# Performance work log

Measured on AMD Instinct MI355X. Metric: run time of the kernel, lower is better.

## Reference

```python
import jax, jax.numpy as jnp
import numpy as np

N = 100000   # nodes
E = 1600000  # edges (before self-loops)
F_IN = 128
H = 64
G = 512      # graphs in batch


def _add_self_loops(edge_index, n):
    loop = jnp.arange(n, dtype=edge_index.dtype)
    src = jnp.concatenate([edge_index[0], loop])
    dst = jnp.concatenate([edge_index[1], loop])
    return src, dst


def _gcn_norm(src, dst, n):
    # PyG GCNConv: deg over targets with self-loops, norm = d^-1/2[src]*d^-1/2[dst]
    deg = jax.ops.segment_sum(jnp.ones_like(dst, dtype=jnp.float32), dst, num_segments=n)
    dinv = jnp.where(deg > 0, jax.lax.rsqrt(deg), 0.0)
    return dinv[src] * dinv[dst]


def _gcn_conv(x, src, dst, norm, W, b):
    xw = x @ W                                # [N, H]
    msg = xw[src] * norm[:, None]             # [E+N, H] gather + scale
    out = jax.ops.segment_sum(msg, dst, num_segments=x.shape[0])
    return out + b


def setup_inputs() -> dict:
    key = jax.random.key(0)
    ks = jax.random.split(key, 9)
    x = jax.random.normal(ks[0], (N, F_IN), dtype=jnp.float32)
    edge_index = jax.random.randint(ks[1], (2, E), 0, N, dtype=jnp.int32)
    batch = jnp.sort(jax.random.randint(ks[2], (N,), 0, G, dtype=jnp.int32))
    s1 = 1.0 / np.sqrt(F_IN)
    s2 = 1.0 / np.sqrt(H)
    W1 = jax.random.uniform(ks[3], (F_IN, H), jnp.float32, -s1, s1)
    b1 = jnp.zeros((H,), jnp.float32)
    W2 = jax.random.uniform(ks[4], (H, H), jnp.float32, -s2, s2)
    b2 = jnp.zeros((H,), jnp.float32)
    Wl = jax.random.uniform(ks[5], (H, 1), jnp.float32, -s2, s2)
    bl = jnp.zeros((1,), jnp.float32)
    return {"x": x, "edge_index": edge_index, "batch": batch,
            "W1": W1, "b1": b1, "W2": W2, "b2": b2, "Wl": Wl, "bl": bl}


def reference(x, edge_index, batch, W1, b1, W2, b2, Wl, bl):
    n = x.shape[0]
    src, dst = _add_self_loops(edge_index, n)
    norm = _gcn_norm(src, dst, n)
    h = jax.nn.relu(_gcn_conv(x, src, dst, norm, W1, b1))
    h = jax.nn.relu(_gcn_conv(h, src, dst, norm, W2, b2))
    # global mean pool over graphs
    sums = jax.ops.segment_sum(h, batch, num_segments=G)          # [G, H]
    cnt = jax.ops.segment_sum(jnp.ones((n,), jnp.float32), batch, num_segments=G)
    pooled = sums / jnp.maximum(cnt, 1.0)[:, None]
    return jax.nn.sigmoid(pooled @ Wl + bl)                        # [G, 1]
```

## Files before the change

### kernel.cpp

```cpp
#include <hip/hip_runtime.h>
#include <hip/hip_bf16.h>
#include <cmath>

#define F_IN 128
#define HDIM 64
#define NPB 256
#define NB1 1024

typedef __attribute__((ext_vector_type(8))) short bf16x8;
typedef __attribute__((ext_vector_type(4))) float f32x4;

__device__ __forceinline__ float bf2f(unsigned short u) {
    union { unsigned int i; float f; } v; v.i = ((unsigned int)u) << 16; return v.f;
}
__device__ __forceinline__ unsigned short f2bf(float f) {
    __hip_bfloat16 h = __float2bfloat16(f);
    union { __hip_bfloat16 h; unsigned short u; } c; c.h = h; return c.u;
}


__launch_bounds__(256)
__global__ void p0_count(const int* __restrict__ dst, int* __restrict__ blk_cnt,
                         int E, int nbuk, int chunk) {
    __shared__ int hist[512];
    int tid = threadIdx.x;
    for (int i = tid; i < nbuk; i += 256) hist[i] = 0;
    __syncthreads();
    int lo = blockIdx.x * chunk;
    int hi = min(E, lo + chunk);
    for (int e = lo + tid; e < hi; e += 256)
        atomicAdd(&hist[dst[e] >> 8], 1);
    __syncthreads();
    for (int i = tid; i < nbuk; i += 256)
        blk_cnt[i * NB1 + blockIdx.x] = hist[i];
}

__launch_bounds__(256)
__global__ void p_scan_blocks(int* __restrict__ blk_cnt, int* __restrict__ bucket_cnt) {
    __shared__ int sd[256];
    int b = blockIdx.x, tid = threadIdx.x;
    int4* row = (int4*)(blk_cnt + (size_t)b * NB1);
    int4 v = row[tid];
    int s0 = v.x, s1 = s0 + v.y, s2 = s1 + v.z, s3 = s2 + v.w;
    sd[tid] = s3;
    __syncthreads();
    for (int off = 1; off < 256; off <<= 1) {
        int a = (tid >= off) ? sd[tid - off] : 0;
        __syncthreads();
        sd[tid] += a;
        __syncthreads();
    }
    int base = sd[tid] - s3;
    int4 o;
    o.x = base; o.y = base + s0; o.z = base + s1; o.w = base + s2;
    row[tid] = o;
    if (tid == 255) bucket_cnt[b] = sd[255];
}

__global__ void p0_scan(const int* __restrict__ cnt, int* __restrict__ base, int nbuk) {
    __shared__ int sd[512];
    int tid = threadIdx.x;
    int v = (tid < nbuk) ? cnt[tid] : 0;
    sd[tid] = v;
    __syncthreads();
    for (int off = 1; off < 512; off <<= 1) {
        int a = (tid >= off) ? sd[tid - off] : 0;
        __syncthreads();
        sd[tid] += a;
        __syncthreads();
    }
    if (tid < nbuk) base[tid] = sd[tid] - v;
    if (tid == nbuk - 1) base[nbuk] = sd[tid];
}

__launch_bounds__(256)
__global__ void p1_place(const int* __restrict__ src, const int* __restrict__ dst,
                         const int* __restrict__ blk_cnt, const int* __restrict__ bucket_base,
                         int* __restrict__ pairs, int E, int nbuk, int chunk) {
    __shared__ int cur[512];
    int tid = threadIdx.x;
    for (int i = tid; i < nbuk; i += 256)
        cur[i] = bucket_base[i] + blk_cnt[i * NB1 + blockIdx.x];
    __syncthreads();
    int lo = blockIdx.x * chunk;
    int hi = min(E, lo + chunk);
    for (int e = lo + tid; e < hi; e += 256) {
        int d = dst[e];
        int pos = atomicAdd(&cur[d >> 8], 1);
        pairs[pos] = (src[e] << 8) | (d & 255);
    }
}

__launch_bounds__(256)
__global__ void p2_csr(const int* __restrict__ pairs, const int* __restrict__ base,
                       float* __restrict__ dinv, int* __restrict__ col,
                       int4* __restrict__ slot_hdr, int n) {
    __shared__ int dl[256];
    __shared__ int sc[256];
    __shared__ int cur[256];
    __shared__ int h64[64];
    __shared__ int s64[64];
    int b = blockIdx.x, tid = threadIdx.x;
    int nlo = b << 8;
    int eb = base[b], ee = base[b + 1];
    dl[tid] = 0;
    if (tid < 64) h64[tid] = 0;
    __syncthreads();
    for (int e = eb + tid; e < ee; e += 256)
        atomicAdd(&dl[pairs[e] & 255], 1);
    __syncthreads();
    int d0 = dl[tid];
    sc[tid] = d0;
    __syncthreads();
    for (int off = 1; off < 256; off <<= 1) {
        int a = (tid >= off) ? sc[tid - off] : 0;
        __syncthreads();
        sc[tid] += a;
        __syncthreads();
    }
    int excl = sc[tid] - d0;
    int node = nlo + tid;
    float dv = rsqrtf((float)(d0 + 1));
    if (node < n) dinv[node] = dv;
    cur[tid] = eb + excl;
    int bin = min(d0, 63);
    atomicAdd(&h64[bin], 1);
    __syncthreads();
    if (tid == 0) { int run = 0; for (int i = 0; i < 64; ++i) { s64[i] = run; run += h64[i]; } }
    __syncthreads();
    if (tid < 64) h64[tid] = 0;
    __syncthreads();
    int pos = s64[bin] + atomicAdd(&h64[bin], 1);
    int4 hdr;
    hdr.x = (node < n) ? node : 0x7fffffff;
    hdr.y = eb + excl;
    hdr.z = d0;
    hdr.w = __float_as_int(dv);
    slot_hdr[nlo + pos] = hdr;
    for (int e = eb + tid; e < ee; e += 256) {
        unsigned int v = (unsigned int)pairs[e];
        int p = atomicAdd(&cur[v & 255], 1);
        col[p] = (int)(v >> 8);
    }
}


__global__ void graph_bounds(const int* __restrict__ batch, int* __restrict__ gstart,
                             int n, int G) {
    int g = blockIdx.x * blockDim.x + threadIdx.x;
    if (g > G) return;
    int lo = 0, hi = n;
    while (lo < hi) {
        int mid = (lo + hi) >> 1;
        if (batch[mid] < g) lo = mid + 1; else hi = mid;
    }
    gstart[g] = lo;
}


__global__ void transpose_w(const float* __restrict__ W, unsigned short* __restrict__ Wt,
                            int K) {
    int t = blockIdx.x * 256 + threadIdx.x;
    if (t >= K * 64) return;
    int c = t & 63, k = t >> 6;
    Wt[c * K + k] = f2bf(W[t]);
}


template <int K>
__launch_bounds__(256)
__global__ void matmul_mfma(const float* __restrict__ X, const unsigned short* __restrict__ Wt,
                            const float* __restrict__ dinv, unsigned short* __restrict__ out,
                            int n) {
    constexpr int KS  = K / 32;
    constexpr int LDX = K + 8;
    __shared__ unsigned short Xs[64 * LDX];
    __shared__ unsigned short Ws[64 * LDX];

    int tid = threadIdx.x;
    int rowbase = blockIdx.x * 64;

    for (int i = tid; i < 64 * (K / 8); i += 256) {
        int r = i / (K / 8), ch = i % (K / 8);
        *(bf16x8*)(Ws + r * LDX + ch * 8) = ((const bf16x8*)Wt)[i];
    }
    {
        const float4* X4 = (const float4*)X;
        for (int i = tid; i < 64 * (K / 4); i += 256) {
            int r = i / (K / 4), k4 = i % (K / 4);
            ushort4 u = { 0, 0, 0, 0 };
            int gr = rowbase + r;
            if (gr < n) {
                float4 v = X4[(size_t)gr * (K / 4) + k4];
                u.x = f2bf(v.x); u.y = f2bf(v.y); u.z = f2bf(v.z); u.w = f2bf(v.w);
            }
            *(ushort4*)(Xs + r * LDX + k4 * 4) = u;
        }
    }
    __syncthreads();

    int wave = tid >> 6, lane = tid & 63;
    int q = lane >> 4, nn = lane & 15;

    f32x4 acc[4] = {{0,0,0,0},{0,0,0,0},{0,0,0,0},{0,0,0,0}};
    int mrow = wave * 16 + nn;
#pragma unroll
    for (int s = 0; s < KS; ++s) {
        bf16x8 af = *(const bf16x8*)(Xs + mrow * LDX + s * 32 + q * 8);
#pragma unroll
        for (int c = 0; c < 4; ++c) {
            bf16x8 bf = *(const bf16x8*)(Ws + (c * 16 + nn) * LDX + s * 32 + q * 8);
            acc[c] = __builtin_amdgcn_mfma_f32_16x16x32_bf16(af, bf, acc[c], 0, 0, 0);
        }
    }

#pragma unroll
    for (int r = 0; r < 4; ++r) {
        int row = rowbase + wave * 16 + q * 4 + r;
        if (row >= n) continue;
        float dv = dinv[row];
#pragma unroll
        for (int c = 0; c < 4; ++c)
            out[(size_t)row * HDIM + c * 16 + nn] = f2bf(acc[c][r] * dv);
    }
}


__launch_bounds__(256)
__global__ void matmul_mfma_b16(const unsigned short* __restrict__ X,
                                const unsigned short* __restrict__ Wt,
                                const float* __restrict__ dinv, unsigned short* __restrict__ out,
                                int n) {
    constexpr int K = 64, KS = 2, LDX = K + 8;
    __shared__ unsigned short Xs[64 * LDX];
    __shared__ unsigned short Ws[64 * LDX];

    int tid = threadIdx.x;
    int rowbase = blockIdx.x * 64;

    for (int i = tid; i < 64 * (K / 8); i += 256) {
        int r = i / (K / 8), ch = i % (K / 8);
        *(bf16x8*)(Ws + r * LDX + ch * 8) = ((const bf16x8*)Wt)[i];
    }
    for (int i = tid; i < 64 * 8; i += 256) {
        int r = i >> 3, c = i & 7;
        int gr = rowbase + r;
        bf16x8 u;
        if (gr < n) u = ((const bf16x8*)X)[(size_t)gr * 8 + c];
        else { short z[8] = {0,0,0,0,0,0,0,0}; u = *(bf16x8*)z; }
        *(bf16x8*)(Xs + r * LDX + c * 8) = u;
    }
    __syncthreads();

    int wave = tid >> 6, lane = tid & 63;
    int q = lane >> 4, nn = lane & 15;

    f32x4 acc[4] = {{0,0,0,0},{0,0,0,0},{0,0,0,0},{0,0,0,0}};
    int mrow = wave * 16 + nn;
#pragma unroll
    for (int s = 0; s < KS; ++s) {
        bf16x8 af = *(const bf16x8*)(Xs + mrow * LDX + s * 32 + q * 8);
#pragma unroll
        for (int c = 0; c < 4; ++c) {
            bf16x8 bf = *(const bf16x8*)(Ws + (c * 16 + nn) * LDX + s * 32 + q * 8);
            acc[c] = __builtin_amdgcn_mfma_f32_16x16x32_bf16(af, bf, acc[c], 0, 0, 0);
        }
    }

#pragma unroll
    for (int r = 0; r < 4; ++r) {
        int row = rowbase + wave * 16 + q * 4 + r;
        if (row >= n) continue;
        float dv = dinv[row];
#pragma unroll
        for (int c = 0; c < 4; ++c)
            out[(size_t)row * HDIM + c * 16 + nn] = f2bf(acc[c][r] * dv);
    }
}


template <bool OUT_BF16>
__launch_bounds__(256)
__global__ void csr_gather8(const int4* __restrict__ slot_hdr, const int* __restrict__ col,
                            const bf16x8* __restrict__ xws, const float* __restrict__ bias,
                            void* __restrict__ outv, int nslots, int n) {
    int t = blockIdx.x * 256 + threadIdx.x;
    int slot = t >> 3;
    if (slot >= nslots) return;
    int L = t & 7;
    int4 hdr = slot_hdr[slot];
    int node = hdr.x;
    if (node >= n) return;
    int s = hdr.y;
    int end = s + hdr.z;
    float dv = __int_as_float(hdr.w);

    bf16x8 sv = xws[(size_t)node * 8 + L];
    float a[8];
#pragma unroll
    for (int j = 0; j < 8; ++j) a[j] = bf2f((unsigned short)sv[j]);

    int e = s;
    for (; e + 4 <= end; e += 4) {
        int c0 = col[e], c1 = col[e + 1], c2 = col[e + 2], c3 = col[e + 3];
        bf16x8 v0 = xws[(size_t)c0 * 8 + L];
        bf16x8 v1 = xws[(size_t)c1 * 8 + L];
        bf16x8 v2 = xws[(size_t)c2 * 8 + L];
        bf16x8 v3 = xws[(size_t)c3 * 8 + L];
#pragma unroll
        for (int j = 0; j < 8; ++j)
            a[j] += (bf2f((unsigned short)v0[j]) + bf2f((unsigned short)v1[j])) +
                    (bf2f((unsigned short)v2[j]) + bf2f((unsigned short)v3[j]));
    }
    for (; e < end; ++e) {
        int c = col[e];
        bf16x8 v = xws[(size_t)c * 8 + L];
#pragma unroll
        for (int j = 0; j < 8; ++j) a[j] += bf2f((unsigned short)v[j]);
    }

    int f0 = L * 8;
    float r[8];
#pragma unroll
    for (int j = 0; j < 8; ++j)
        r[j] = fmaxf(fmaf(a[j], dv, bias[f0 + j]), 0.0f);

    if (OUT_BF16) {
        bf16x8 o;
#pragma unroll
        for (int j = 0; j < 8; ++j) o[j] = (short)f2bf(r[j]);
        ((bf16x8*)outv)[(size_t)node * 8 + L] = o;
    } else {
        float4* op = (float4*)outv + (size_t)node * 16 + L * 2;
        op[0] = make_float4(r[0], r[1], r[2], r[3]);
        op[1] = make_float4(r[4], r[5], r[6], r[7]);
    }
}


__launch_bounds__(256)
__global__ void pool_head(const unsigned short* __restrict__ h, const int* __restrict__ gstart,
                          const float* __restrict__ Wl, const float* __restrict__ bl,
                          float* __restrict__ out, int G) {
    int g = blockIdx.x;
    int s = gstart[g], e = gstart[g + 1];
    int f  = threadIdx.x & 63;
    int rg = threadIdx.x >> 6;
    float acc = 0.0f;
    for (int i = s + rg; i < e; i += 4)
        acc += bf2f(h[(size_t)i * HDIM + f]);
    __shared__ float red[4][HDIM];
    red[rg][f] = acc;
    __syncthreads();
    if (rg == 0) {
        float v = (red[0][f] + red[1][f]) + (red[2][f] + red[3][f]);
        float c = fmaxf((float)(e - s), 1.0f);
        v = v * Wl[f] * (1.0f / c);
#pragma unroll
        for (int off = 32; off; off >>= 1) v += __shfl_down(v, off, 64);
        if (f == 0) out[g] = 1.0f / (1.0f + expf(-(v + bl[0])));
    }
}


extern "C" void kernel_launch(void* const* d_in, const int* in_sizes, int n_in,
                              void* d_out, int out_size, void* d_ws, size_t ws_size,
                              hipStream_t stream) {
    const float* x   = (const float*)d_in[0];
    const int* ei    = (const int*)d_in[1];
    const int* batch = (const int*)d_in[2];
    const float* W1  = (const float*)d_in[3];
    const float* b1  = (const float*)d_in[4];
    const float* W2  = (const float*)d_in[5];
    const float* b2  = (const float*)d_in[6];
    const float* Wl  = (const float*)d_in[7];
    const float* bl  = (const float*)d_in[8];
    float* out = (float*)d_out;

    const int n = in_sizes[0] / F_IN;
    const int E = in_sizes[1] / 2;
    const int G = out_size;

    const int* srcp = ei;
    const int* dstp = ei + E;

    int nbuk = (n + NPB - 1) / NPB;
    int nslots = nbuk * NPB;

    char* wsb = (char*)d_ws;
    auto alloc = [&](size_t bytes) { char* p = wsb; wsb += (bytes + 255) & ~(size_t)255; return p; };
    float* dinv       = (float*)alloc((size_t)n * 4);
    int4*  slot_hdr   = (int4*)alloc((size_t)nslots * 16);
    int*   bucket_cnt = (int*)alloc(512 * 4);
    int*   bucket_base= (int*)alloc(513 * 4);
    int*   blk_cnt    = (int*)alloc((size_t)nbuk * NB1 * 4);
    int*   pairs      = (int*)alloc((size_t)E * 4);
    int*   colx       = (int*)alloc((size_t)E * 4);
    unsigned short* w1t  = (unsigned short*)alloc((size_t)F_IN * HDIM * 2);
    unsigned short* w2t  = (unsigned short*)alloc((size_t)HDIM * HDIM * 2);
    unsigned short* xwsb = (unsigned short*)alloc((size_t)n * HDIM * 2);
    unsigned short* xh1  = (unsigned short*)alloc((size_t)n * HDIM * 2);
    unsigned short* xh2  = (unsigned short*)alloc((size_t)n * HDIM * 2);
    int*   gstart     = (int*)alloc(((size_t)G + 1) * 4);

    const int TB = 256;
    int gMM  = (n + 63) / 64;
    int chunk = (E + NB1 - 1) / NB1;
    int gG8  = (nslots * 8 + TB - 1) / TB;

    transpose_w<<<(F_IN * 64 + 255) / 256, 256, 0, stream>>>(W1, w1t, F_IN);
    transpose_w<<<(HDIM * 64 + 255) / 256, 256, 0, stream>>>(W2, w2t, HDIM);

    p0_count<<<NB1, TB, 0, stream>>>(dstp, blk_cnt, E, nbuk, chunk);
    p_scan_blocks<<<nbuk, TB, 0, stream>>>(blk_cnt, bucket_cnt);
    p0_scan<<<1, 512, 0, stream>>>(bucket_cnt, bucket_base, nbuk);
    p1_place<<<NB1, TB, 0, stream>>>(srcp, dstp, blk_cnt, bucket_base, pairs, E, nbuk, chunk);
    p2_csr<<<nbuk, TB, 0, stream>>>(pairs, bucket_base, dinv, colx, slot_hdr, n);
    graph_bounds<<<(G + 1 + TB - 1) / TB, TB, 0, stream>>>(batch, gstart, n, G);

    matmul_mfma<F_IN><<<gMM, 256, 0, stream>>>(x, w1t, dinv, xwsb, n);
    csr_gather8<true><<<gG8, TB, 0, stream>>>(slot_hdr, colx, (const bf16x8*)xwsb,
                                              b1, xh1, nslots, n);

    matmul_mfma_b16<<<gMM, 256, 0, stream>>>(xh1, w2t, dinv, xwsb, n);
    csr_gather8<true><<<gG8, TB, 0, stream>>>(slot_hdr, colx, (const bf16x8*)xwsb,
                                              b2, xh2, nslots, n);

    pool_head<<<G, 256, 0, stream>>>(xh2, gstart, Wl, bl, out, G);
}
```

Measured before the change: 280.5 us.

## Store scaled XW features in FP8 to halve gather traffic; merge small launches

The matmul kernels now write the dinv-scaled XW rows as FP8 (one byte per feature) instead of bf16. The CSR gather kernels read 8-byte FP8 vectors and convert them with packed cvt instructions into fp32 accumulators, which halves the random-gather bytes per edge. Separately, the two weight-transpose launches are merged into one, and graph_bounds is folded into the bucket-scan kernel, removing launches. FP8 quantization of the messages lowers numerical precision and may push the output past the tolerance.

```diff
diff --git a/kernel.cpp b/kernel.cpp
--- a/kernel.cpp
+++ b/kernel.cpp
@@ -9,6 +9,7 @@
 
 typedef __attribute__((ext_vector_type(8))) short bf16x8;
 typedef __attribute__((ext_vector_type(4))) float f32x4;
+typedef __attribute__((ext_vector_type(2))) float f32x2;
 
 __device__ __forceinline__ float bf2f(unsigned short u) {
     union { unsigned int i; float f; } v; v.i = ((unsigned int)u) << 16; return v.f;
@@ -16,6 +17,17 @@
 __device__ __forceinline__ unsigned short f2bf(float f) {
     __hip_bfloat16 h = __float2bfloat16(f);
     union { __hip_bfloat16 h; unsigned short u; } c; c.h = h; return c.u;
+}
+__device__ __forceinline__ unsigned char f2fp8(float f) {
+    int p = __builtin_amdgcn_cvt_pk_fp8_f32(f, f, 0, false);
+    return (unsigned char)(p & 0xff);
+}
+__device__ __forceinline__ void fp8x8_acc(uint2 v, float* a) {
+    f32x2 f;
+    f = __builtin_amdgcn_cvt_pk_f32_fp8(v.x, false); a[0] += f.x; a[1] += f.y;
+    f = __builtin_amdgcn_cvt_pk_f32_fp8(v.x, true);  a[2] += f.x; a[3] += f.y;
+    f = __builtin_amdgcn_cvt_pk_f32_fp8(v.y, false); a[4] += f.x; a[5] += f.y;
+    f = __builtin_amdgcn_cvt_pk_f32_fp8(v.y, true);  a[6] += f.x; a[7] += f.y;
 }
 
 
@@ -57,20 +69,33 @@
     if (tid == 255) bucket_cnt[b] = sd[255];
 }
 
-__global__ void p0_scan(const int* __restrict__ cnt, int* __restrict__ base, int nbuk) {
-    __shared__ int sd[512];
-    int tid = threadIdx.x;
-    int v = (tid < nbuk) ? cnt[tid] : 0;
-    sd[tid] = v;
-    __syncthreads();
-    for (int off = 1; off < 512; off <<= 1) {
-        int a = (tid >= off) ? sd[tid - off] : 0;
+__global__ void scan_bounds(const int* __restrict__ cnt, int* __restrict__ base, int nbuk,
+                            const int* __restrict__ batch, int* __restrict__ gstart,
+                            int n, int G) {
+    if (blockIdx.x == 0) {
+        __shared__ int sd[512];
+        int tid = threadIdx.x;
+        int v = (tid < nbuk) ? cnt[tid] : 0;
+        sd[tid] = v;
         __syncthreads();
-        sd[tid] += a;
-        __syncthreads();
-    }
-    if (tid < nbuk) base[tid] = sd[tid] - v;
-    if (tid == nbuk - 1) base[nbuk] = sd[tid];
+        for (int off = 1; off < 512; off <<= 1) {
+            int a = (tid >= off) ? sd[tid - off] : 0;
+            __syncthreads();
+            sd[tid] += a;
+            __syncthreads();
+        }
+        if (tid < nbuk) base[tid] = sd[tid] - v;
+        if (tid == nbuk - 1) base[nbuk] = sd[tid];
+    } else {
+        int g = (blockIdx.x - 1) * 512 + threadIdx.x;
+        if (g > G) return;
+        int lo = 0, hi = n;
+        while (lo < hi) {
+            int mid = (lo + hi) >> 1;
+            if (batch[mid] < g) lo = mid + 1; else hi = mid;
+        }
+        gstart[g] = lo;
+    }
 }
 
 __launch_bounds__(256)
@@ -145,32 +170,26 @@
 }
 
 
-__global__ void graph_bounds(const int* __restrict__ batch, int* __restrict__ gstart,
-                             int n, int G) {
-    int g = blockIdx.x * blockDim.x + threadIdx.x;
-    if (g > G) return;
-    int lo = 0, hi = n;
-    while (lo < hi) {
-        int mid = (lo + hi) >> 1;
-        if (batch[mid] < g) lo = mid + 1; else hi = mid;
-    }
-    gstart[g] = lo;
-}
-
-
-__global__ void transpose_w(const float* __restrict__ W, unsigned short* __restrict__ Wt,
-                            int K) {
+__global__ void transpose_both(const float* __restrict__ W1, const float* __restrict__ W2,
+                               unsigned short* __restrict__ w1t, unsigned short* __restrict__ w2t) {
     int t = blockIdx.x * 256 + threadIdx.x;
-    if (t >= K * 64) return;
-    int c = t & 63, k = t >> 6;
-    Wt[c * K + k] = f2bf(W[t]);
+    if (t < F_IN * 64) {
+        int c = t & 63, k = t >> 6;
+        w1t[c * F_IN + k] = f2bf(W1[t]);
+    } else {
+        int u = t - F_IN * 64;
+        if (u < HDIM * 64) {
+            int c = u & 63, k = u >> 6;
+            w2t[c * HDIM + k] = f2bf(W2[u]);
+        }
+    }
 }
 
 
 template <int K>
 __launch_bounds__(256)
 __global__ void matmul_mfma(const float* __restrict__ X, const unsigned short* __restrict__ Wt,
-                            const float* __restrict__ dinv, unsigned short* __restrict__ out,
+                            const float* __restrict__ dinv, unsigned char* __restrict__ out,
                             int n) {
     constexpr int KS  = K / 32;
     constexpr int LDX = K + 8;
@@ -221,7 +240,7 @@
         float dv = dinv[row];
 #pragma unroll
         for (int c = 0; c < 4; ++c)
-            out[(size_t)row * HDIM + c * 16 + nn] = f2bf(acc[c][r] * dv);
+            out[(size_t)row * HDIM + c * 16 + nn] = f2fp8(acc[c][r] * dv);
     }
 }
 
@@ -229,7 +248,7 @@
 __launch_bounds__(256)
 __global__ void matmul_mfma_b16(const unsigned short* __restrict__ X,
                                 const unsigned short* __restrict__ Wt,
-                                const float* __restrict__ dinv, unsigned short* __restrict__ out,
+                                const float* __restrict__ dinv, unsigned char* __restrict__ out,
                                 int n) {
     constexpr int K = 64, KS = 2, LDX = K + 8;
     __shared__ unsigned short Xs[64 * LDX];
@@ -274,16 +293,15 @@
         float dv = dinv[row];
 #pragma unroll
         for (int c = 0; c < 4; ++c)
-            out[(size_t)row * HDIM + c * 16 + nn] = f2bf(acc[c][r] * dv);
-    }
-}
-
-
-template <bool OUT_BF16>
-__launch_bounds__(256)
-__global__ void csr_gather8(const int4* __restrict__ slot_hdr, const int* __restrict__ col,
-                            const bf16x8* __restrict__ xws, const float* __restrict__ bias,
-                            void* __restrict__ outv, int nslots, int n) {
+            out[(size_t)row * HDIM + c * 16 + nn] = f2fp8(acc[c][r] * dv);
+    }
+}
+
+
+__launch_bounds__(256)
+__global__ void csr_gather8_fp8(const int4* __restrict__ slot_hdr, const int* __restrict__ col,
+                                const uint2* __restrict__ xws, const float* __restrict__ bias,
+                                bf16x8* __restrict__ outb, int nslots, int n) {
     int t = blockIdx.x * 256 + threadIdx.x;
     int slot = t >> 3;
     if (slot >= nslots) return;
@@ -295,46 +313,27 @@
     int end = s + hdr.z;
     float dv = __int_as_float(hdr.w);
 
-    bf16x8 sv = xws[(size_t)node * 8 + L];
-    float a[8];
-#pragma unroll
-    for (int j = 0; j < 8; ++j) a[j] = bf2f((unsigned short)sv[j]);
+    float a[8] = {0, 0, 0, 0, 0, 0, 0, 0};
+    fp8x8_acc(xws[(size_t)node * 8 + L], a);
 
     int e = s;
     for (; e + 4 <= end; e += 4) {
         int c0 = col[e], c1 = col[e + 1], c2 = col[e + 2], c3 = col[e + 3];
-        bf16x8 v0 = xws[(size_t)c0 * 8 + L];
-        bf16x8 v1 = xws[(size_t)c1 * 8 + L];
-        bf16x8 v2 = xws[(size_t)c2 * 8 + L];
-        bf16x8 v3 = xws[(size_t)c3 * 8 + L];
-#pragma unroll
-        for (int j = 0; j < 8; ++j)
-            a[j] += (bf2f((unsigned short)v0[j]) + bf2f((unsigned short)v1[j])) +
-                    (bf2f((unsigned short)v2[j]) + bf2f((unsigned short)v3[j]));
-    }
-    for (; e < end; ++e) {
-        int c = col[e];
-        bf16x8 v = xws[(size_t)c * 8 + L];
-#pragma unroll
-        for (int j = 0; j < 8; ++j) a[j] += bf2f((unsigned short)v[j]);
-    }
+        uint2 v0 = xws[(size_t)c0 * 8 + L];
+        uint2 v1 = xws[(size_t)c1 * 8 + L];
+        uint2 v2 = xws[(size_t)c2 * 8 + L];
+        uint2 v3 = xws[(size_t)c3 * 8 + L];
+        fp8x8_acc(v0, a); fp8x8_acc(v1, a); fp8x8_acc(v2, a); fp8x8_acc(v3, a);
+    }
+    for (; e < end; ++e)
+        fp8x8_acc(xws[(size_t)col[e] * 8 + L], a);
 
     int f0 = L * 8;
-    float r[8];
+    bf16x8 o;
 #pragma unroll
     for (int j = 0; j < 8; ++j)
-        r[j] = fmaxf(fmaf(a[j], dv, bias[f0 + j]), 0.0f);
-
-    if (OUT_BF16) {
-        bf16x8 o;
-#pragma unroll
-        for (int j = 0; j < 8; ++j) o[j] = (short)f2bf(r[j]);
-        ((bf16x8*)outv)[(size_t)node * 8 + L] = o;
-    } else {
-        float4* op = (float4*)outv + (size_t)node * 16 + L * 2;
-        op[0] = make_float4(r[0], r[1], r[2], r[3]);
-        op[1] = make_float4(r[4], r[5], r[6], r[7]);
-    }
+        o[j] = (short)f2bf(fmaxf(fmaf(a[j], dv, bias[f0 + j]), 0.0f));
+    outb[(size_t)node * 8 + L] = o;
 }
 
 
@@ -398,7 +397,7 @@
     int*   colx       = (int*)alloc((size_t)E * 4);
     unsigned short* w1t  = (unsigned short*)alloc((size_t)F_IN * HDIM * 2);
     unsigned short* w2t  = (unsigned short*)alloc((size_t)HDIM * HDIM * 2);
-    unsigned short* xwsb = (unsigned short*)alloc((size_t)n * HDIM * 2);
+    unsigned char*  xws8 = (unsigned char*)alloc((size_t)n * HDIM);
     unsigned short* xh1  = (unsigned short*)alloc((size_t)n * HDIM * 2);
     unsigned short* xh2  = (unsigned short*)alloc((size_t)n * HDIM * 2);
     int*   gstart     = (int*)alloc(((size_t)G + 1) * 4);
@@ -408,23 +407,20 @@
     int chunk = (E + NB1 - 1) / NB1;
     int gG8  = (nslots * 8 + TB - 1) / TB;
 
-    transpose_w<<<(F_IN * 64 + 255) / 256, 256, 0, stream>>>(W1, w1t, F_IN);
-    transpose_w<<<(HDIM * 64 + 255) / 256, 256, 0, stream>>>(W2, w2t, HDIM);
-
+    transpose_both<<<(F_IN * 64 + HDIM * 64 + 255) / 256, 256, 0, stream>>>(W1, W2, w1t, w2t);
     p0_count<<<NB1, TB, 0, stream>>>(dstp, blk_cnt, E, nbuk, chunk);
     p_scan_blocks<<<nbuk, TB, 0, stream>>>(blk_cnt, bucket_cnt);
-    p0_scan<<<1, 512, 0, stream>>>(bucket_cnt, bucket_base, nbuk);
+    scan_bounds<<<3, 512, 0, stream>>>(bucket_cnt, bucket_base, nbuk, batch, gstart, n, G);
     p1_place<<<NB1, TB, 0, stream>>>(srcp, dstp, blk_cnt, bucket_base, pairs, E, nbuk, chunk);
     p2_csr<<<nbuk, TB, 0, stream>>>(pairs, bucket_base, dinv, colx, slot_hdr, n);
-    graph_bounds<<<(G + 1 + TB - 1) / TB, TB, 0, stream>>>(batch, gstart, n, G);
-
-    matmul_mfma<F_IN><<<gMM, 256, 0, stream>>>(x, w1t, dinv, xwsb, n);
-    csr_gather8<true><<<gG8, TB, 0, stream>>>(slot_hdr, colx, (const bf16x8*)xwsb,
-                                              b1, xh1, nslots, n);
-
-    matmul_mfma_b16<<<gMM, 256, 0, stream>>>(xh1, w2t, dinv, xwsb, n);
-    csr_gather8<true><<<gG8, TB, 0, stream>>>(slot_hdr, colx, (const bf16x8*)xwsb,
-                                              b2, xh2, nslots, n);
+
+    matmul_mfma<F_IN><<<gMM, 256, 0, stream>>>(x, w1t, dinv, xws8, n);
+    csr_gather8_fp8<<<gG8, TB, 0, stream>>>(slot_hdr, colx, (const uint2*)xws8,
+                                            b1, (bf16x8*)xh1, nslots, n);
+
+    matmul_mfma_b16<<<gMM, 256, 0, stream>>>(xh1, w2t, dinv, xws8, n);
+    csr_gather8_fp8<<<gG8, TB, 0, stream>>>(slot_hdr, colx, (const uint2*)xws8,
+                                            b2, (bf16x8*)xh2, nslots, n);
 
     pool_head<<<G, 256, 0, stream>>>(xh2, gstart, Wl, bl, out, G);
 }
```

Result: faster. 254.6 us (-9.2%).
